# Performance work log

Measured on AMD Instinct MI355X. Metric: run time of the kernel, lower is better.

The kernel has to match this reference:

```python
import jax, jax.numpy as jnp
import numpy as np

INPUT_DIM, HIDDEN_DIM, N_HEADS, N_AGENTS = 256, 512, 8, 64
BATCH, N_ENTITIES = 128, 256


def setup_inputs() -> dict:
    key = jax.random.key(0)
    ks = jax.random.split(key, 6)
    x = jax.random.normal(ks[0], (BATCH, N_ENTITIES, INPUT_DIM), dtype=jnp.float32)
    # encode: LeakyReLU -> Linear(input_dim, hidden_dim)
    W_enc = jax.random.normal(ks[1], (INPUT_DIM, HIDDEN_DIM), dtype=jnp.float32) * (1.0 / np.sqrt(INPUT_DIM))
    b_enc = jnp.zeros((HIDDEN_DIM,), dtype=jnp.float32)
    # per-head full hidden x hidden projections, stacked on head axis
    WQ = jax.random.normal(ks[2], (N_HEADS, HIDDEN_DIM, HIDDEN_DIM), dtype=jnp.float32)
    WK = jax.random.normal(ks[3], (N_HEADS, HIDDEN_DIM, HIDDEN_DIM), dtype=jnp.float32)
    WV = jax.random.normal(ks[4], (N_HEADS, HIDDEN_DIM, HIDDEN_DIM), dtype=jnp.float32)
    return {"x": x, "W_enc": W_enc, "b_enc": b_enc, "WQ": WQ, "WK": WK, "WV": WV, "n_agents": N_AGENTS}


def reference(x, W_enc, b_enc, WQ, WK, WV, n_agents):
    scale = 1.0 / np.sqrt(WQ.shape[-1]).astype(np.float32)
    # encode: LeakyReLU(0.01) then Linear
    h = jax.nn.leaky_relu(x, negative_slope=0.01) @ W_enc + b_enc  # [b, e, H]
    ha = h[:, :n_agents]  # [b, a, H]
    # all heads at once: n = head axis
    Q = jnp.einsum('bah,nhd->nbad', ha, WQ)
    K = jnp.einsum('beh,nhd->nbed', h, WK)
    V = jnp.einsum('beh,nhd->nbed', h, WV)
    scores = jnp.einsum('nbad,nbed->nbae', Q, K) * scale
    p = jax.nn.softmax(scores, axis=-1)
    # redundant renormalization from the original code
    prob = p / (jnp.sum(p, axis=-1, keepdims=True) + 1e-12)
    z = jnp.einsum('nbae,nbed->nbad', prob, V)  # [n, b, a, H]
    return jnp.mean(z, axis=0)  # [b, a, H]
```

## Files before the change

### kernel.cpp

```cpp
#include <hip/hip_runtime.h>
#include <math.h>

#define BATCH  128
#define NENT   256
#define INDIM  256
#define HID    512
#define NHEAD  8
#define NAGENT 64
#define SCALE  0.04419417382415922f

typedef unsigned short u16;
typedef unsigned int   u32;

typedef __bf16 bf16x8  __attribute__((ext_vector_type(8)));
typedef float  floatx4 __attribute__((ext_vector_type(4)));
typedef u32    u32x4   __attribute__((ext_vector_type(4)));
typedef u32    u32x2   __attribute__((ext_vector_type(2)));

union Frag {
    u32x4 s;
    struct { u32x2 lo, hi; } p;
    bf16x8 v;
};

__device__ __forceinline__ u16 f2bf(float x) {
    u32 u = __float_as_uint(x);
    return (u16)((u + 0x7FFFu + ((u >> 16) & 1u)) >> 16);
}
__device__ __forceinline__ float bf2f(u16 b) {
    return __uint_as_float(((u32)b) << 16);
}
__device__ __forceinline__ void split4(const float4& r, ushort4& hh, ushort4& hl) {
    hh.x = f2bf(r.x); hl.x = f2bf(r.x - bf2f(hh.x));
    hh.y = f2bf(r.y); hl.y = f2bf(r.y - bf2f(hh.y));
    hh.z = f2bf(r.z); hl.z = f2bf(r.z - bf2f(hh.z));
    hh.w = f2bf(r.w); hl.w = f2bf(r.w - bf2f(hh.w));
}

__global__ __launch_bounds__(256) void wenc_t_kernel(const float* __restrict__ W,
                                                     u16* __restrict__ Wt_h,
                                                     u16* __restrict__ Wt_l) {
    __shared__ float tile[64][68];
    const int bid = blockIdx.x;
    const int k0 = (bid & 3) * 64;
    const int d0 = (bid >> 2) * 64;
    const int t = threadIdx.x;
    const int ki = t >> 2, dc = (t & 3) * 16;
    #pragma unroll
    for (int c = 0; c < 4; ++c)
        *(float4*)&tile[ki][dc + c * 4] =
            *(const float4*)(W + (size_t)(k0 + ki) * HID + d0 + dc + c * 4);
    __syncthreads();
    const int dr = t >> 2, kc = (t & 3) * 16;
    #pragma unroll
    for (int c = 0; c < 4; ++c) {
        float4 v = make_float4(tile[kc + c * 4 + 0][dr], tile[kc + c * 4 + 1][dr],
                               tile[kc + c * 4 + 2][dr], tile[kc + c * 4 + 3][dr]);
        ushort4 hh, hl; split4(v, hh, hl);
        size_t o = (size_t)(d0 + dr) * INDIM + k0 + kc + c * 4;
        *(ushort4*)(Wt_h + o) = hh;
        *(ushort4*)(Wt_l + o) = hl;
    }
}

__global__ __launch_bounds__(256) void enc_kernel(const float* __restrict__ x,
                                                  const u16* __restrict__ Wt_h,
                                                  const u16* __restrict__ Wt_l,
                                                  const float* __restrict__ bias,
                                                  u16* __restrict__ h_h,
                                                  u16* __restrict__ h_l) {
    __shared__ u16 Ah[32][264];
    __shared__ u16 Al[32][264];
    const int r0 = blockIdx.x * 32;
    const int t  = threadIdx.x;
    {
        const int row = t >> 3;
        const float* xr = x + (size_t)(r0 + row) * INDIM;
        #pragma unroll
        for (int j = 0; j < 8; ++j) {
            const int k0 = ((t & 7) + j * 8) * 4;
            float4 v = *(const float4*)(xr + k0);
            v.x = v.x > 0.f ? v.x : 0.01f * v.x;
            v.y = v.y > 0.f ? v.y : 0.01f * v.y;
            v.z = v.z > 0.f ? v.z : 0.01f * v.z;
            v.w = v.w > 0.f ? v.w : 0.01f * v.w;
            ushort4 hh, hl; split4(v, hh, hl);
            *(ushort4*)&Ah[row][k0] = hh;
            *(ushort4*)&Al[row][k0] = hl;
        }
    }
    __syncthreads();

    const int wid = t >> 6, lane = t & 63, l15 = lane & 15, quad = lane >> 4;
    const int mbase = (wid & 1) * 16;
    const int nbase = (wid >> 1) * 256;
    const floatx4 z4 = {0.f, 0.f, 0.f, 0.f};
    floatx4 acc[16];
    #pragma unroll
    for (int i = 0; i < 16; ++i) acc[i] = z4;

    for (int ks = 0; ks < 8; ++ks) {
        const int k = ks * 32 + quad * 8;
        Frag Afh, Afl;
        Afh.s = *(const u32x4*)&Ah[mbase + l15][k];
        Afl.s = *(const u32x4*)&Al[mbase + l15][k];
        #pragma unroll
        for (int nt = 0; nt < 16; ++nt) {
            const int d = nbase + nt * 16 + l15;
            Frag Bh, Bl;
            Bh.s = *(const u32x4*)(Wt_h + (size_t)d * INDIM + k);
            Bl.s = *(const u32x4*)(Wt_l + (size_t)d * INDIM + k);
            floatx4 c = acc[nt];
            c = __builtin_amdgcn_mfma_f32_16x16x32_bf16(Afh.v, Bh.v, c, 0, 0, 0);
            c = __builtin_amdgcn_mfma_f32_16x16x32_bf16(Afh.v, Bl.v, c, 0, 0, 0);
            c = __builtin_amdgcn_mfma_f32_16x16x32_bf16(Afl.v, Bh.v, c, 0, 0, 0);
            acc[nt] = c;
        }
    }
    #pragma unroll
    for (int nt = 0; nt < 16; ++nt) {
        const int d = nbase + nt * 16 + l15;
        const float bv = bias[d];
        #pragma unroll
        for (int r = 0; r < 4; ++r) {
            const float v = acc[nt][r] + bv;
            const u16 hi = f2bf(v);
            const u16 lo = f2bf(v - bf2f(hi));
            const size_t o = (size_t)(r0 + mbase + quad * 4 + r) * HID + d;
            h_h[o] = hi;
            h_l[o] = lo;
        }
    }
}

__global__ __launch_bounds__(256) void wqk_kernel(const float* __restrict__ WQ,
                                                  const float* __restrict__ WK,
                                                  u16* __restrict__ Mt_h,
                                                  u16* __restrict__ Mt_l) {
    __shared__ u16 Ah[64][72], Al[64][72], Bh[64][72], Bl[64][72];
    const int bid = blockIdx.x;
    const int jt = (bid & 7) * 64;
    const int it = ((bid >> 3) & 7) * 64;
    const int n  = bid >> 6;
    const float* qp = WQ + (size_t)n * 262144;
    const float* kp = WK + (size_t)n * 262144;
    const int t = threadIdx.x;
    const int wid = t >> 6, lane = t & 63, l15 = lane & 15, quad = lane >> 4;
    const int srow = t >> 2, sc = (t & 3) * 16;

    const floatx4 z4 = {0.f, 0.f, 0.f, 0.f};
    floatx4 acc[4];
    #pragma unroll
    for (int i = 0; i < 4; ++i) acc[i] = z4;

    for (int kc = 0; kc < HID; kc += 64) {
        #pragma unroll
        for (int f = 0; f < 4; ++f) {
            float4 va = *(const float4*)(kp + (size_t)(jt + srow) * HID + kc + sc + f * 4);
            ushort4 hh, hl; split4(va, hh, hl);
            *(ushort4*)&Ah[srow][sc + f * 4] = hh;
            *(ushort4*)&Al[srow][sc + f * 4] = hl;
            float4 vb = *(const float4*)(qp + (size_t)(it + srow) * HID + kc + sc + f * 4);
            split4(vb, hh, hl);
            *(ushort4*)&Bh[srow][sc + f * 4] = hh;
            *(ushort4*)&Bl[srow][sc + f * 4] = hl;
        }
        __syncthreads();
        #pragma unroll
        for (int ks = 0; ks < 2; ++ks) {
            const int k = ks * 32 + quad * 8;
            Frag Afh, Afl;
            Afh.s = *(const u32x4*)&Ah[wid * 16 + l15][k];
            Afl.s = *(const u32x4*)&Al[wid * 16 + l15][k];
            #pragma unroll
            for (int nt = 0; nt < 4; ++nt) {
                Frag Bfh, Bfl;
                Bfh.s = *(const u32x4*)&Bh[nt * 16 + l15][k];
                Bfl.s = *(const u32x4*)&Bl[nt * 16 + l15][k];
                floatx4 c = acc[nt];
                c = __builtin_amdgcn_mfma_f32_16x16x32_bf16(Afh.v, Bfh.v, c, 0, 0, 0);
                c = __builtin_amdgcn_mfma_f32_16x16x32_bf16(Afh.v, Bfl.v, c, 0, 0, 0);
                c = __builtin_amdgcn_mfma_f32_16x16x32_bf16(Afl.v, Bfh.v, c, 0, 0, 0);
                acc[nt] = c;
            }
        }
        __syncthreads();
    }
    #pragma unroll
    for (int nt = 0; nt < 4; ++nt)
        #pragma unroll
        for (int r = 0; r < 4; ++r) {
            const float v = acc[nt][r] * SCALE;
            const u16 hi = f2bf(v);
            const u16 lo = f2bf(v - bf2f(hi));
            const int j = jt + wid * 16 + quad * 4 + r;
            const int i = it + nt * 16 + l15;
            const size_t o = (size_t)n * 262144 + (size_t)j * HID + i;
            Mt_h[o] = hi;
            Mt_l[o] = lo;
        }
}

__global__ __launch_bounds__(256) void wvt_kernel(const float* __restrict__ WV,
                                                  u16* __restrict__ WVt) {
    __shared__ float tile[64][68];
    const int bid = blockIdx.x;
    const int i0 = (bid & 7) * 64;
    const int o0 = ((bid >> 3) & 7) * 64;
    const int n  = bid >> 6;
    const float* src = WV + (size_t)n * 262144;
    const int t  = threadIdx.x;
    const int di = t >> 2;
    const int dc = (t & 3) * 16;
    #pragma unroll
    for (int c = 0; c < 4; ++c)
        *(float4*)&tile[di][dc + c * 4] =
            *(const float4*)(src + (size_t)(i0 + di) * HID + o0 + dc + c * 4);
    __syncthreads();
    const int dr = t >> 2;
    const int ic = (t & 3) * 16;
    size_t o = (size_t)n * 262144 + (size_t)(o0 + dr) * HID + i0 + ic;
    #pragma unroll
    for (int c = 0; c < 4; ++c) {
        ushort4 v = make_ushort4(f2bf(tile[ic + c * 4 + 0][dr]), f2bf(tile[ic + c * 4 + 1][dr]),
                                 f2bf(tile[ic + c * 4 + 2][dr]), f2bf(tile[ic + c * 4 + 3][dr]));
        *(ushort4*)(WVt + o + c * 4) = v;
    }
}

__global__ __launch_bounds__(256, 3) void attn_kernel(const u16* __restrict__ h_h,
                                                      const u16* __restrict__ h_l,
                                                      const u16* __restrict__ Mt_h,
                                                      const u16* __restrict__ Mt_l,
                                                      const u16* __restrict__ WVt,
                                                      float* __restrict__ out) {
    __shared__ __align__(16) char SM[53504];
    u16*   Th  = (u16*)SM;
    u16*   Tl  = (u16*)(SM + 16640);
    float* S   = (float*)SM;
    float* red = (float*)(SM + 33792);
    u16*   HbT = (u16*)SM;
    u16*   U   = (u16*)SM;
    u16*   Pt  = (u16*)(SM + 36864);

    const int bid = blockIdx.x;
    const int x7 = bid & 7;
    const int s  = bid >> 3;
    const int at = s & 1;
    const int n  = (x7 >> 1) | (((s >> 1) & 1) << 2);
    const int b  = ((s >> 2) << 1) | (x7 & 1);

    const int tid  = threadIdx.x;
    const int wid  = tid >> 6;
    const int lane = tid & 63;
    const int l15  = lane & 15;
    const int quad = lane >> 4;

    const u16* Mth = Mt_h + (size_t)n * 262144;
    const u16* Mtl = Mt_l + (size_t)n * 262144;
    const u16* Wv  = WVt  + (size_t)n * 262144;
    const size_t hb_base = (size_t)b * NENT * HID;
    const size_t ha_base = hb_base + (size_t)at * 32 * HID;

    const floatx4 z4 = {0.f, 0.f, 0.f, 0.f};
    floatx4 Sacc[8];
    #pragma unroll
    for (int i = 0; i < 8; ++i) Sacc[i] = z4;

    for (int H = 0; H < 2; ++H) {
        floatx4 Tacc[8];
        #pragma unroll
        for (int i = 0; i < 8; ++i) Tacc[i] = z4;
        for (int ks = 0; ks < 16; ++ks) {
            const int k = ks * 32 + quad * 8;
            Frag Ahf[2], Alf[2];
            #pragma unroll
            for (int mt = 0; mt < 2; ++mt) {
                const size_t ro = ha_base + (size_t)(mt * 16 + l15) * HID + k;
                Ahf[mt].s = *(const u32x4*)(h_h + ro);
                Alf[mt].s = *(const u32x4*)(h_l + ro);
            }
            #pragma unroll
            for (int nt = 0; nt < 4; ++nt) {
                const int d = H * 256 + (wid * 4 + nt) * 16 + l15;
                Frag Bh, Bl;
                Bh.s = *(const u32x4*)(Mth + (size_t)d * HID + k);
                Bl.s = *(const u32x4*)(Mtl + (size_t)d * HID + k);
                #pragma unroll
                for (int mt = 0; mt < 2; ++mt) {
                    floatx4 c = Tacc[mt * 4 + nt];
                    c = __builtin_amdgcn_mfma_f32_16x16x32_bf16(Ahf[mt].v, Bh.v, c, 0, 0, 0);
                    c = __builtin_amdgcn_mfma_f32_16x16x32_bf16(Ahf[mt].v, Bl.v, c, 0, 0, 0);
                    c = __builtin_amdgcn_mfma_f32_16x16x32_bf16(Alf[mt].v, Bh.v, c, 0, 0, 0);
                    Tacc[mt * 4 + nt] = c;
                }
            }
        }
        __syncthreads();
        #pragma unroll
        for (int mt = 0; mt < 2; ++mt)
            #pragma unroll
            for (int nt = 0; nt < 4; ++nt)
                #pragma unroll
                for (int r = 0; r < 4; ++r) {
                    const float v = Tacc[mt * 4 + nt][r];
                    const int a  = mt * 16 + quad * 4 + r;
                    const int dl = (wid * 4 + nt) * 16 + l15;
                    const u16 hi = f2bf(v);
                    Th[a * 260 + dl] = hi;
                    Tl[a * 260 + dl] = f2bf(v - bf2f(hi));
                }
        __syncthreads();
        for (int ks = 0; ks < 8; ++ks) {
            const int kl = ks * 32 + quad * 8;
            const int kg = H * 256 + kl;
            Frag Ahf[4], Alf[4];
            #pragma unroll
            for (int mt = 0; mt < 4; ++mt) {
                const size_t ro = hb_base + (size_t)((wid * 4 + mt) * 16 + l15) * HID + kg;
                Ahf[mt].s = *(const u32x4*)(h_h + ro);
                Alf[mt].s = *(const u32x4*)(h_l + ro);
            }
            #pragma unroll
            for (int nt = 0; nt < 2; ++nt) {
                const int ac = nt * 16 + l15;
                Frag Bh, Bl;
                Bh.p.lo = *(const u32x2*)(Th + ac * 260 + kl);
                Bh.p.hi = *(const u32x2*)(Th + ac * 260 + kl + 4);
                Bl.p.lo = *(const u32x2*)(Tl + ac * 260 + kl);
                Bl.p.hi = *(const u32x2*)(Tl + ac * 260 + kl + 4);
                #pragma unroll
                for (int mt = 0; mt < 4; ++mt) {
                    floatx4 c = Sacc[mt * 2 + nt];
                    c = __builtin_amdgcn_mfma_f32_16x16x32_bf16(Ahf[mt].v, Bh.v, c, 0, 0, 0);
                    c = __builtin_amdgcn_mfma_f32_16x16x32_bf16(Ahf[mt].v, Bl.v, c, 0, 0, 0);
                    c = __builtin_amdgcn_mfma_f32_16x16x32_bf16(Alf[mt].v, Bh.v, c, 0, 0, 0);
                    Sacc[mt * 2 + nt] = c;
                }
            }
        }
    }
    __syncthreads();
    #pragma unroll
    for (int mt = 0; mt < 4; ++mt)
        #pragma unroll
        for (int nt = 0; nt < 2; ++nt)
            #pragma unroll
            for (int r = 0; r < 4; ++r) {
                const int e = (wid * 4 + mt) * 16 + quad * 4 + r;
                const int a = nt * 16 + l15;
                S[e * 33 + a] = Sacc[mt * 2 + nt][r];
            }
    __syncthreads();
    {
        const int a   = tid & 31;
        const int seg = tid >> 5;
        float v[32];
        #pragma unroll
        for (int i = 0; i < 32; ++i) v[i] = S[(seg * 32 + i) * 33 + a];
        float mx = v[0];
        #pragma unroll
        for (int i = 1; i < 32; ++i) mx = fmaxf(mx, v[i]);
        red[a * 8 + seg] = mx;
        __syncthreads();
        float gmx = red[a * 8 + 0];
        #pragma unroll
        for (int i = 1; i < 8; ++i) gmx = fmaxf(gmx, red[a * 8 + i]);
        __syncthreads();
        float sum = 0.f;
        #pragma unroll
        for (int i = 0; i < 32; ++i) { v[i] = expf(v[i] - gmx); sum += v[i]; }
        red[a * 8 + seg] = sum;
        __syncthreads();
        float tot = 0.f;
        #pragma unroll
        for (int i = 0; i < 8; ++i) tot += red[a * 8 + i];
        const float inv = 1.0f / tot;
        #pragma unroll
        for (int i = 0; i < 32; ++i)
            Pt[a * 260 + seg * 32 + i] = f2bf(v[i] * inv);
    }
    __syncthreads();
    floatx4 Uacc[16];
    #pragma unroll
    for (int i = 0; i < 16; ++i) Uacc[i] = z4;
    const int d0w = wid * 128;
    u32* Hb32 = (u32*)HbT;
    for (int et = 0; et < 8; ++et) {
        {
            const int ep = lane & 15;
            const int q  = lane >> 4;
            const size_t r0 = hb_base + (size_t)(et * 32 + 2 * ep) * HID;
            #pragma unroll
            for (int c = 0; c < 4; ++c) {
                const int d0 = d0w + c * 32 + q * 8;
                u32x4 u0 = *(const u32x4*)(h_h + r0 + d0);
                u32x4 u1 = *(const u32x4*)(h_h + r0 + HID + d0);
                #pragma unroll
                for (int p = 0; p < 4; ++p) {
                    const u32 w0 = (u0[p] & 0xFFFFu) | (u1[p] << 16);
                    const u32 w1 = (u0[p] >> 16) | (u1[p] & 0xFFFF0000u);
                    Hb32[(d0 + 2 * p) * 18 + ep]     = w0;
                    Hb32[(d0 + 2 * p + 1) * 18 + ep] = w1;
                }
            }
        }
        Frag Ap[2];
        #pragma unroll
        for (int mt = 0; mt < 2; ++mt) {
            const int ar = mt * 16 + l15;
            Ap[mt].p.lo = *(const u32x2*)(Pt + ar * 260 + et * 32 + quad * 8);
            Ap[mt].p.hi = *(const u32x2*)(Pt + ar * 260 + et * 32 + quad * 8 + 4);
        }
        #pragma unroll
        for (int dt = 0; dt < 8; ++dt) {
            const int d = d0w + dt * 16 + l15;
            Frag Bf;
            Bf.p.lo = *(const u32x2*)(HbT + d * 36 + quad * 8);
            Bf.p.hi = *(const u32x2*)(HbT + d * 36 + quad * 8 + 4);
            #pragma unroll
            for (int mt = 0; mt < 2; ++mt)
                Uacc[mt * 8 + dt] = __builtin_amdgcn_mfma_f32_16x16x32_bf16(Ap[mt].v, Bf.v, Uacc[mt * 8 + dt], 0, 0, 0);
        }
    }
    __syncthreads();
    #pragma unroll
    for (int mt = 0; mt < 2; ++mt)
        #pragma unroll
        for (int dt = 0; dt < 8; ++dt)
            #pragma unroll
            for (int r = 0; r < 4; ++r) {
                const int a = mt * 16 + quad * 4 + r;
                const int d = d0w + dt * 16 + l15;
                U[a * 520 + d] = f2bf(Uacc[mt * 8 + dt][r]);
            }
    __syncthreads();
    floatx4 Zacc[16];
    #pragma unroll
    for (int i = 0; i < 16; ++i) Zacc[i] = z4;
    for (int ks = 0; ks < 16; ++ks) {
        const int k = ks * 32 + quad * 8;
        Frag Au[2];
        #pragma unroll
        for (int mt = 0; mt < 2; ++mt) {
            Au[mt].p.lo = *(const u32x2*)(U + (mt * 16 + l15) * 520 + k);
            Au[mt].p.hi = *(const u32x2*)(U + (mt * 16 + l15) * 520 + k + 4);
        }
        #pragma unroll
        for (int dt = 0; dt < 8; ++dt) {
            const int dn = (wid * 8 + dt) * 16 + l15;
            Frag Bw;
            Bw.s = *(const u32x4*)(Wv + (size_t)dn * HID + k);
            #pragma unroll
            for (int mt = 0; mt < 2; ++mt)
                Zacc[mt * 8 + dt] = __builtin_amdgcn_mfma_f32_16x16x32_bf16(Au[mt].v, Bw.v, Zacc[mt * 8 + dt], 0, 0, 0);
        }
    }
    float* ob = out + ((size_t)b * NAGENT + at * 32) * HID;
    #pragma unroll
    for (int mt = 0; mt < 2; ++mt)
        #pragma unroll
        for (int dt = 0; dt < 8; ++dt)
            #pragma unroll
            for (int r = 0; r < 4; ++r) {
                const int a  = mt * 16 + quad * 4 + r;
                const int dn = (wid * 8 + dt) * 16 + l15;
                atomicAdd(ob + (size_t)a * HID + dn, Zacc[mt * 8 + dt][r] * 0.125f);
            }
}

extern "C" void kernel_launch(void* const* d_in, const int* in_sizes, int n_in,
                              void* d_out, int out_size, void* d_ws, size_t ws_size,
                              hipStream_t stream) {
    const float* x     = (const float*)d_in[0];
    const float* W_enc = (const float*)d_in[1];
    const float* b_enc = (const float*)d_in[2];
    const float* WQ    = (const float*)d_in[3];
    const float* WK    = (const float*)d_in[4];
    const float* WV    = (const float*)d_in[5];
    float* out = (float*)d_out;

    char* ws = (char*)d_ws;
    u16* h_h  = (u16*)ws;
    u16* h_l  = (u16*)(ws + 33554432);
    u16* Mt_h = (u16*)(ws + 67108864);
    u16* Mt_l = (u16*)(ws + 71303168);
    u16* WVt  = (u16*)(ws + 75497472);
    u16* Wt_h = WVt;
    u16* Wt_l = WVt + 131072;

    hipMemsetAsync(d_out, 0, (size_t)out_size * sizeof(float), stream);
    wenc_t_kernel<<<32, 256, 0, stream>>>(W_enc, Wt_h, Wt_l);
    enc_kernel<<<1024, 256, 0, stream>>>(x, Wt_h, Wt_l, b_enc, h_h, h_l);
    wvt_kernel<<<512, 256, 0, stream>>>(WV, WVt);
    wqk_kernel<<<512, 256, 0, stream>>>(WQ, WK, Mt_h, Mt_l);
    attn_kernel<<<2048, 256, 0, stream>>>(h_h, h_l, Mt_h, Mt_l, WVt, out);
}
```

Baseline: 984.2 us.

## Double-buffer global operand loads and pretranspose h for the P·H stage

Adds register double-buffering (prefetch of the next k-step's fragments) to the Q·M, S, and U·WV GEMM loops in the attention kernel so global loads overlap MFMA work. Also adds a separate kernel that transposes h once into a workspace buffer, letting the P·H stage read B fragments directly instead of repacking h into shared memory every tile. The transpose path only runs when the workspace is large enough. Doubling the buffered fragments raises register pressure, which under launch_bounds(256,3) may cause spills.

```diff
diff --git a/kernel.cpp b/kernel.cpp
--- a/kernel.cpp
+++ b/kernel.cpp
@@ -130,6 +130,31 @@
             h_h[o] = hi;
             h_l[o] = lo;
         }
+    }
+}
+
+__global__ __launch_bounds__(256) void ht_kernel(const u16* __restrict__ h_h,
+                                                 u16* __restrict__ hT) {
+    __shared__ u16 tile[64][72];
+    const int bid = blockIdx.x;
+    const int dt = bid & 7;
+    const int et = (bid >> 3) & 3;
+    const int b  = bid >> 5;
+    const int t  = threadIdx.x;
+    const int r  = t >> 2, cs = (t & 3) * 16;
+    const u16* src = h_h + (size_t)(b * 256 + et * 64 + r) * HID + dt * 64 + cs;
+    *(ushort4*)&tile[r][cs + 0]  = *(const ushort4*)(src + 0);
+    *(ushort4*)&tile[r][cs + 4]  = *(const ushort4*)(src + 4);
+    *(ushort4*)&tile[r][cs + 8]  = *(const ushort4*)(src + 8);
+    *(ushort4*)&tile[r][cs + 12] = *(const ushort4*)(src + 12);
+    __syncthreads();
+    const int d = t >> 2, es = (t & 3) * 16;
+    u16* dst = hT + (size_t)b * 131072 + (size_t)(dt * 64 + d) * 256 + et * 64 + es;
+    #pragma unroll
+    for (int c = 0; c < 4; ++c) {
+        ushort4 v = make_ushort4(tile[es + c * 4 + 0][d], tile[es + c * 4 + 1][d],
+                                 tile[es + c * 4 + 2][d], tile[es + c * 4 + 3][d]);
+        *(ushort4*)(dst + c * 4) = v;
     }
 }
 
@@ -228,11 +253,13 @@
     }
 }
 
+template<bool USE_HT>
 __global__ __launch_bounds__(256, 3) void attn_kernel(const u16* __restrict__ h_h,
                                                       const u16* __restrict__ h_l,
                                                       const u16* __restrict__ Mt_h,
                                                       const u16* __restrict__ Mt_l,
                                                       const u16* __restrict__ WVt,
+                                                      const u16* __restrict__ hT,
                                                       float* __restrict__ out) {
     __shared__ __align__(16) char SM[53504];
     u16*   Th  = (u16*)SM;
@@ -259,6 +286,7 @@
     const u16* Mth = Mt_h + (size_t)n * 262144;
     const u16* Mtl = Mt_l + (size_t)n * 262144;
     const u16* Wv  = WVt  + (size_t)n * 262144;
+    const u16* hTb = hT + (size_t)b * 131072;
     const size_t hb_base = (size_t)b * NENT * HID;
     const size_t ha_base = hb_base + (size_t)at * 32 * HID;
 
@@ -271,7 +299,20 @@
         floatx4 Tacc[8];
         #pragma unroll
         for (int i = 0; i < 8; ++i) Tacc[i] = z4;
+        Frag Bh[2][4], Bl[2][4];
+        auto loadBA = [&](int ksv, Frag* bh, Frag* bl) {
+            const int k = ksv * 32 + quad * 8;
+            #pragma unroll
+            for (int nt = 0; nt < 4; ++nt) {
+                const int d = H * 256 + (wid * 4 + nt) * 16 + l15;
+                bh[nt].s = *(const u32x4*)(Mth + (size_t)d * HID + k);
+                bl[nt].s = *(const u32x4*)(Mtl + (size_t)d * HID + k);
+            }
+        };
+        loadBA(0, Bh[0], Bl[0]);
+        #pragma unroll 2
         for (int ks = 0; ks < 16; ++ks) {
+            const int cur = ks & 1, nxt = cur ^ 1;
             const int k = ks * 32 + quad * 8;
             Frag Ahf[2], Alf[2];
             #pragma unroll
@@ -280,21 +321,17 @@
                 Ahf[mt].s = *(const u32x4*)(h_h + ro);
                 Alf[mt].s = *(const u32x4*)(h_l + ro);
             }
-            #pragma unroll
-            for (int nt = 0; nt < 4; ++nt) {
-                const int d = H * 256 + (wid * 4 + nt) * 16 + l15;
-                Frag Bh, Bl;
-                Bh.s = *(const u32x4*)(Mth + (size_t)d * HID + k);
-                Bl.s = *(const u32x4*)(Mtl + (size_t)d * HID + k);
+            if (ks < 15) loadBA(ks + 1, Bh[nxt], Bl[nxt]);
+            #pragma unroll
+            for (int nt = 0; nt < 4; ++nt)
                 #pragma unroll
                 for (int mt = 0; mt < 2; ++mt) {
                     floatx4 c = Tacc[mt * 4 + nt];
-                    c = __builtin_amdgcn_mfma_f32_16x16x32_bf16(Ahf[mt].v, Bh.v, c, 0, 0, 0);
-                    c = __builtin_amdgcn_mfma_f32_16x16x32_bf16(Ahf[mt].v, Bl.v, c, 0, 0, 0);
-                    c = __builtin_amdgcn_mfma_f32_16x16x32_bf16(Alf[mt].v, Bh.v, c, 0, 0, 0);
+                    c = __builtin_amdgcn_mfma_f32_16x16x32_bf16(Ahf[mt].v, Bh[cur][nt].v, c, 0, 0, 0);
+                    c = __builtin_amdgcn_mfma_f32_16x16x32_bf16(Ahf[mt].v, Bl[cur][nt].v, c, 0, 0, 0);
+                    c = __builtin_amdgcn_mfma_f32_16x16x32_bf16(Alf[mt].v, Bh[cur][nt].v, c, 0, 0, 0);
                     Tacc[mt * 4 + nt] = c;
                 }
-            }
         }
         __syncthreads();
         #pragma unroll
@@ -311,30 +348,36 @@
                     Tl[a * 260 + dl] = f2bf(v - bf2f(hi));
                 }
         __syncthreads();
-        for (int ks = 0; ks < 8; ++ks) {
-            const int kl = ks * 32 + quad * 8;
-            const int kg = H * 256 + kl;
-            Frag Ahf[4], Alf[4];
+        Frag Ahb[2][4], Alb[2][4];
+        auto loadAB2 = [&](int ksv, Frag* ah, Frag* al) {
+            const int kg = H * 256 + ksv * 32 + quad * 8;
             #pragma unroll
             for (int mt = 0; mt < 4; ++mt) {
                 const size_t ro = hb_base + (size_t)((wid * 4 + mt) * 16 + l15) * HID + kg;
-                Ahf[mt].s = *(const u32x4*)(h_h + ro);
-                Alf[mt].s = *(const u32x4*)(h_l + ro);
-            }
+                ah[mt].s = *(const u32x4*)(h_h + ro);
+                al[mt].s = *(const u32x4*)(h_l + ro);
+            }
+        };
+        loadAB2(0, Ahb[0], Alb[0]);
+        #pragma unroll 2
+        for (int ks = 0; ks < 8; ++ks) {
+            const int cur = ks & 1, nxt = cur ^ 1;
+            const int kl = ks * 32 + quad * 8;
+            if (ks < 7) loadAB2(ks + 1, Ahb[nxt], Alb[nxt]);
             #pragma unroll
             for (int nt = 0; nt < 2; ++nt) {
                 const int ac = nt * 16 + l15;
-                Frag Bh, Bl;
-                Bh.p.lo = *(const u32x2*)(Th + ac * 260 + kl);
-                Bh.p.hi = *(const u32x2*)(Th + ac * 260 + kl + 4);
-                Bl.p.lo = *(const u32x2*)(Tl + ac * 260 + kl);
-                Bl.p.hi = *(const u32x2*)(Tl + ac * 260 + kl + 4);
+                Frag Bfh, Bfl;
+                Bfh.p.lo = *(const u32x2*)(Th + ac * 260 + kl);
+                Bfh.p.hi = *(const u32x2*)(Th + ac * 260 + kl + 4);
+                Bfl.p.lo = *(const u32x2*)(Tl + ac * 260 + kl);
+                Bfl.p.hi = *(const u32x2*)(Tl + ac * 260 + kl + 4);
                 #pragma unroll
                 for (int mt = 0; mt < 4; ++mt) {
                     floatx4 c = Sacc[mt * 2 + nt];
-                    c = __builtin_amdgcn_mfma_f32_16x16x32_bf16(Ahf[mt].v, Bh.v, c, 0, 0, 0);
-                    c = __builtin_amdgcn_mfma_f32_16x16x32_bf16(Ahf[mt].v, Bl.v, c, 0, 0, 0);
-                    c = __builtin_amdgcn_mfma_f32_16x16x32_bf16(Alf[mt].v, Bh.v, c, 0, 0, 0);
+                    c = __builtin_amdgcn_mfma_f32_16x16x32_bf16(Ahb[cur][mt].v, Bfh.v, c, 0, 0, 0);
+                    c = __builtin_amdgcn_mfma_f32_16x16x32_bf16(Ahb[cur][mt].v, Bfl.v, c, 0, 0, 0);
+                    c = __builtin_amdgcn_mfma_f32_16x16x32_bf16(Alb[cur][mt].v, Bfh.v, c, 0, 0, 0);
                     Sacc[mt * 2 + nt] = c;
                 }
             }
@@ -385,42 +428,71 @@
     #pragma unroll
     for (int i = 0; i < 16; ++i) Uacc[i] = z4;
     const int d0w = wid * 128;
-    u32* Hb32 = (u32*)HbT;
-    for (int et = 0; et < 8; ++et) {
-        {
-            const int ep = lane & 15;
-            const int q  = lane >> 4;
-            const size_t r0 = hb_base + (size_t)(et * 32 + 2 * ep) * HID;
-            #pragma unroll
-            for (int c = 0; c < 4; ++c) {
-                const int d0 = d0w + c * 32 + q * 8;
-                u32x4 u0 = *(const u32x4*)(h_h + r0 + d0);
-                u32x4 u1 = *(const u32x4*)(h_h + r0 + HID + d0);
+    if (USE_HT) {
+        Frag Bc[2][8];
+        auto loadBC = [&](int etv, Frag* bc) {
+            #pragma unroll
+            for (int dt = 0; dt < 8; ++dt) {
+                const int d = d0w + dt * 16 + l15;
+                bc[dt].s = *(const u32x4*)(hTb + (size_t)d * 256 + etv * 32 + quad * 8);
+            }
+        };
+        loadBC(0, Bc[0]);
+        #pragma unroll 2
+        for (int et = 0; et < 8; ++et) {
+            const int cur = et & 1, nxt = cur ^ 1;
+            if (et < 7) loadBC(et + 1, Bc[nxt]);
+            Frag Ap[2];
+            #pragma unroll
+            for (int mt = 0; mt < 2; ++mt) {
+                const int ar = mt * 16 + l15;
+                Ap[mt].p.lo = *(const u32x2*)(Pt + ar * 260 + et * 32 + quad * 8);
+                Ap[mt].p.hi = *(const u32x2*)(Pt + ar * 260 + et * 32 + quad * 8 + 4);
+            }
+            #pragma unroll
+            for (int dt = 0; dt < 8; ++dt)
                 #pragma unroll
-                for (int p = 0; p < 4; ++p) {
-                    const u32 w0 = (u0[p] & 0xFFFFu) | (u1[p] << 16);
-                    const u32 w1 = (u0[p] >> 16) | (u1[p] & 0xFFFF0000u);
-                    Hb32[(d0 + 2 * p) * 18 + ep]     = w0;
-                    Hb32[(d0 + 2 * p + 1) * 18 + ep] = w1;
+                for (int mt = 0; mt < 2; ++mt)
+                    Uacc[mt * 8 + dt] = __builtin_amdgcn_mfma_f32_16x16x32_bf16(Ap[mt].v, Bc[cur][dt].v, Uacc[mt * 8 + dt], 0, 0, 0);
+        }
+    } else {
+        u32* Hb32 = (u32*)HbT;
+        for (int et = 0; et < 8; ++et) {
+            {
+                const int ep = lane & 15;
+                const int q  = lane >> 4;
+                const size_t r0 = hb_base + (size_t)(et * 32 + 2 * ep) * HID;
+                #pragma unroll
+                for (int c = 0; c < 4; ++c) {
+                    const int d0 = d0w + c * 32 + q * 8;
+                    u32x4 u0 = *(const u32x4*)(h_h + r0 + d0);
+                    u32x4 u1 = *(const u32x4*)(h_h + r0 + HID + d0);
+                    #pragma unroll
+                    for (int p = 0; p < 4; ++p) {
+                        const u32 w0 = (u0[p] & 0xFFFFu) | (u1[p] << 16);
+                        const u32 w1 = (u0[p] >> 16) | (u1[p] & 0xFFFF0000u);
+                        Hb32[(d0 + 2 * p) * 18 + ep]     = w0;
+                        Hb32[(d0 + 2 * p + 1) * 18 + ep] = w1;
+                    }
                 }
             }
-        }
-        Frag Ap[2];
-        #pragma unroll
-        for (int mt = 0; mt < 2; ++mt) {
-            const int ar = mt * 16 + l15;
-            Ap[mt].p.lo = *(const u32x2*)(Pt + ar * 260 + et * 32 + quad * 8);
-            Ap[mt].p.hi = *(const u32x2*)(Pt + ar * 260 + et * 32 + quad * 8 + 4);
-        }
-        #pragma unroll
-        for (int dt = 0; dt < 8; ++dt) {
-            const int d = d0w + dt * 16 + l15;
-            Frag Bf;
-            Bf.p.lo = *(const u32x2*)(HbT + d * 36 + quad * 8);
-            Bf.p.hi = *(const u32x2*)(HbT + d * 36 + quad * 8 + 4);
-            #pragma unroll
-            for (int mt = 0; mt < 2; ++mt)
-                Uacc[mt * 8 + dt] = __builtin_amdgcn_mfma_f32_16x16x32_bf16(Ap[mt].v, Bf.v, Uacc[mt * 8 + dt], 0, 0, 0);
+            Frag Ap[2];
+            #pragma unroll
+            for (int mt = 0; mt < 2; ++mt) {
+                const int ar = mt * 16 + l15;
+                Ap[mt].p.lo = *(const u32x2*)(Pt + ar * 260 + et * 32 + quad * 8);
+                Ap[mt].p.hi = *(const u32x2*)(Pt + ar * 260 + et * 32 + quad * 8 + 4);
+            }
+            #pragma unroll
+            for (int dt = 0; dt < 8; ++dt) {
+                const int d = d0w + dt * 16 + l15;
+                Frag Bf;
+                Bf.p.lo = *(const u32x2*)(HbT + d * 36 + quad * 8);
+                Bf.p.hi = *(const u32x2*)(HbT + d * 36 + quad * 8 + 4);
+                #pragma unroll
+                for (int mt = 0; mt < 2; ++mt)
+                    Uacc[mt * 8 + dt] = __builtin_amdgcn_mfma_f32_16x16x32_bf16(Ap[mt].v, Bf.v, Uacc[mt * 8 + dt], 0, 0, 0);
+            }
         }
     }
     __syncthreads();
@@ -438,7 +510,19 @@
     floatx4 Zacc[16];
     #pragma unroll
     for (int i = 0; i < 16; ++i) Zacc[i] = z4;
+    Frag Bw[2][8];
+    auto loadBD = [&](int ksv, Frag* bw) {
+        const int k = ksv * 32 + quad * 8;
+        #pragma unroll
+        for (int dt = 0; dt < 8; ++dt) {
+            const int dn = (wid * 8 + dt) * 16 + l15;
+            bw[dt].s = *(const u32x4*)(Wv + (size_t)dn * HID + k);
+        }
+    };
+    loadBD(0, Bw[0]);
+    #pragma unroll 2
     for (int ks = 0; ks < 16; ++ks) {
+        const int cur = ks & 1, nxt = cur ^ 1;
         const int k = ks * 32 + quad * 8;
         Frag Au[2];
         #pragma unroll
@@ -446,15 +530,12 @@
             Au[mt].p.lo = *(const u32x2*)(U + (mt * 16 + l15) * 520 + k);
             Au[mt].p.hi = *(const u32x2*)(U + (mt * 16 + l15) * 520 + k + 4);
         }
-        #pragma unroll
-        for (int dt = 0; dt < 8; ++dt) {
-            const int dn = (wid * 8 + dt) * 16 + l15;
-            Frag Bw;
-            Bw.s = *(const u32x4*)(Wv + (size_t)dn * HID + k);
+        if (ks < 15) loadBD(ks + 1, Bw[nxt]);
+        #pragma unroll
+        for (int dt = 0; dt < 8; ++dt)
             #pragma unroll
             for (int mt = 0; mt < 2; ++mt)
-                Zacc[mt * 8 + dt] = __builtin_amdgcn_mfma_f32_16x16x32_bf16(Au[mt].v, Bw.v, Zacc[mt * 8 + dt], 0, 0, 0);
-        }
+                Zacc[mt * 8 + dt] = __builtin_amdgcn_mfma_f32_16x16x32_bf16(Au[mt].v, Bw[cur][dt].v, Zacc[mt * 8 + dt], 0, 0, 0);
     }
     float* ob = out + ((size_t)b * NAGENT + at * 32) * HID;
     #pragma unroll
@@ -486,13 +567,20 @@
     u16* Mt_h = (u16*)(ws + 67108864);
     u16* Mt_l = (u16*)(ws + 71303168);
     u16* WVt  = (u16*)(ws + 75497472);
+    u16* hT   = (u16*)(ws + 79691776);
     u16* Wt_h = WVt;
     u16* Wt_l = WVt + 131072;
+
+    const bool useHT = ws_size >= (size_t)113246208;
 
     hipMemsetAsync(d_out, 0, (size_t)out_size * sizeof(float), stream);
     wenc_t_kernel<<<32, 256, 0, stream>>>(W_enc, Wt_h, Wt_l);
     enc_kernel<<<1024, 256, 0, stream>>>(x, Wt_h, Wt_l, b_enc, h_h, h_l);
+    if (useHT) ht_kernel<<<4096, 256, 0, stream>>>(h_h, hT);
     wvt_kernel<<<512, 256, 0, stream>>>(WV, WVt);
     wqk_kernel<<<512, 256, 0, stream>>>(WQ, WK, Mt_h, Mt_l);
-    attn_kernel<<<2048, 256, 0, stream>>>(h_h, h_l, Mt_h, Mt_l, WVt, out);
-}
+    if (useHT)
+        attn_kernel<true><<<2048, 256, 0, stream>>>(h_h, h_l, Mt_h, Mt_l, WVt, hT, out);
+    else
+        attn_kernel<false><<<2048, 256, 0, stream>>>(h_h, h_l, Mt_h, Mt_l, WVt, hT, out);
+}
```

Result: no change. 989.2 us (+0.5%).
